# Performance work log

Hardware: AMD Instinct MI355X
Metric: run time of the kernel (lower is better)

Reference implementation:

```python
import jax, jax.numpy as jnp
import numpy as np

C = 128      # in_channels == out_channels
K = 3        # kernel_size
PAD = 1
DIL = 1
EPS = 1e-5


def setup_inputs() -> dict:
    key = jax.random.key(0)
    ks = jax.random.split(key, 6)
    B, L = 8, 16384
    x = jax.random.normal(ks[0], (B, C, L), jnp.float32)
    # depthwise Conv1d(C, C, K, groups=C), bias=True (nn.Conv1d default)
    dw_w = jax.random.normal(ks[1], (C, 1, K), jnp.float32) * (1.0 / np.sqrt(K))
    dw_b = jax.random.normal(ks[2], (C,), jnp.float32) * 0.05
    # LayerNorm(C)
    ln_g = jnp.ones((C,), jnp.float32)
    ln_b = jnp.zeros((C,), jnp.float32)
    # offset Linear(C -> groups*K) ; weight stored [out, in] like torch
    off_w = jax.random.normal(ks[3], (K, C), jnp.float32) * 0.02
    off_b = jnp.zeros((K,), jnp.float32)
    # deformable conv weight [C_out, C_in, K], bias=False
    dc_w = jax.random.normal(ks[4], (C, C, K), jnp.float32) * (1.0 / np.sqrt(C * K))
    return dict(x=x, dw_w=dw_w, dw_b=dw_b, ln_g=ln_g, ln_b=ln_b,
                off_w=off_w, off_b=off_b, dc_w=dc_w)


def _forward(x, dw_w, dw_b, ln_g, ln_b, off_w, off_b, dc_w):
    B, _, L = x.shape
    # --- dw_conv: depthwise conv + LayerNorm(channel) + ReLU ---
    y = jax.lax.conv_general_dilated(
        x, dw_w, window_strides=(1,), padding=[(PAD, PAD)],
        dimension_numbers=('NCH', 'OIH', 'NCH'), feature_group_count=C)
    y = y + dw_b[None, :, None]
    yt = y.transpose(0, 2, 1)                      # [B, L, C]
    mu = jnp.mean(yt, axis=-1, keepdims=True)
    var = jnp.mean((yt - mu) ** 2, axis=-1, keepdims=True)
    yn = (yt - mu) * jax.lax.rsqrt(var + EPS) * ln_g + ln_b
    yr = jax.nn.relu(yn)                           # [B, L, C]
    # --- offset linear: [B, L, C] -> [B, L, K] ---
    offset = yr @ off_w.T + off_b                  # [B, L, K]
    # --- deformable conv1d with linear interpolation, zero padding ---
    base = (jnp.arange(L, dtype=x.dtype)[None, :, None]
            + (jnp.arange(K, dtype=x.dtype) * DIL - PAD)[None, None, :])
    pos = base + offset                            # [B, L, K] fractional positions
    p0 = jnp.floor(pos)
    frac = pos - p0                                # [B, L, K]
    p0i = p0.astype(jnp.int32)
    p1i = p0i + 1
    v0 = ((p0i >= 0) & (p0i < L)).astype(x.dtype)
    v1 = ((p1i >= 0) & (p1i < L)).astype(x.dtype)
    i0 = jnp.clip(p0i, 0, L - 1)
    i1 = jnp.clip(p1i, 0, L - 1)
    gather = jax.vmap(lambda xb, ib: xb[:, ib])    # xb [C,L], ib [L,K] -> [C,L,K]
    g0 = gather(x, i0)                             # [B, C, L, K]
    g1 = gather(x, i1)
    g = g0 * ((1.0 - frac) * v0)[:, None] + g1 * (frac * v1)[:, None]
    # weighted sum over input channels and kernel taps
    return jnp.einsum('bclk,ock->bol', g, dc_w)    # [B, C_out, L]


def reference(x, dw_w, dw_b, ln_g, ln_b, off_w, off_b, dc_w):
    return _forward(x, dw_w, dw_b, ln_g, ln_b, off_w, off_b, dc_w)
```

## Files before the change

### kernel.cpp

```cpp
#include <hip/hip_runtime.h>
#include <hip/hip_bf16.h>
#include <cstdint>
#include <cstddef>

#define C_CH 128
#define L_LEN 16384
#define B_N 8
#define K_T 3
#define EPS 1e-5f
#define WPAD 8
#define WIN_G 144

typedef __attribute__((ext_vector_type(8))) short short8;
typedef __attribute__((ext_vector_type(4))) float float4v;

__device__ __forceinline__ short f2bf(float f) {
  union { float f; unsigned u; } v; v.f = f;
  unsigned r = v.u + 0x7fffu + ((v.u >> 16) & 1u);
  return (short)(r >> 16);
}
__device__ __forceinline__ float bflo(unsigned d) {
  union { unsigned u; float f; } v; v.u = d << 16; return v.f;
}
__device__ __forceinline__ float bfhi(unsigned d) {
  union { unsigned u; float f; } v; v.u = d & 0xffff0000u; return v.f;
}
__device__ __forceinline__ unsigned packbf(float a, float b) {
  unsigned ua = __float_as_uint(a) + 0x8000u;
  unsigned ub = __float_as_uint(b) + 0x8000u;
  return (ua >> 16) | (ub & 0xffff0000u);
}
__device__ __forceinline__ int clampL(int v) {
  return v < 0 ? 0 : (v > L_LEN - 1 ? L_LEN - 1 : v);
}
__device__ __forceinline__ void gl_lds16(const void* g, void* l) {
  __builtin_amdgcn_global_load_lds(
      (const __attribute__((address_space(1))) unsigned*)g,
      (__attribute__((address_space(3))) unsigned*)l, 16, 0, 0);
}

__global__ void repack_w2(const float* __restrict__ dc_w, short* __restrict__ Wp2) {
  int tid = blockIdx.x * 256 + threadIdx.x;
  if (tid >= C_CH * C_CH * K_T) return;
  int j = tid & 7;
  int m = (tid >> 3) & 127;
  int qk = (tid >> 10) & 3;
  int ks = tid >> 12;
  int kt = ks >> 2, s = ks & 3;
  int c = qk * 32 + s * 8 + j;
  Wp2[tid] = f2bf(dc_w[(m * C_CH + c) * K_T + kt]);
}

__global__ __launch_bounds__(256, 4) void offsets_k3(
    const float* __restrict__ x,
    const float* __restrict__ dw_w, const float* __restrict__ dw_b,
    const float* __restrict__ ln_g, const float* __restrict__ ln_b,
    const float* __restrict__ off_w, const float* __restrict__ off_b,
    short* __restrict__ xT, unsigned* __restrict__ d_wab, unsigned* __restrict__ d_idx) {
  __shared__ float swt[1152];
  int t = threadIdx.x;
  int b = blockIdx.y;
  int l0 = blockIdx.x * 64;

  for (int i = t; i < 1152; i += 256) {
    float v;
    if (i < 384) v = dw_w[i];
    else if (i < 512) v = dw_b[i - 384];
    else if (i < 640) v = ln_g[i - 512];
    else if (i < 768) v = ln_b[i - 640];
    else v = off_w[i - 768];
    swt[i] = v;
  }
  __syncthreads();

  int l_loc = t >> 2, sub = t & 3;
  int lg = l0 + l_loc;
  float mL = (lg >= 1) ? 1.f : 0.f;
  float mR = (lg + 1 < L_LEN) ? 1.f : 0.f;
  int lgm = lg - 1 < 0 ? 0 : lg - 1;
  int lgp = lg + 1 > L_LEN - 1 ? L_LEN - 1 : lg + 1;
  const float* xb = x + (size_t)b * C_CH * L_LEN;
  const float* xc = xb + (size_t)(sub * 32) * L_LEN;

  float ys[32];
  unsigned xpk[16];
  float sum = 0.f, sumsq = 0.f;
  #pragma unroll
  for (int j = 0; j < 32; ++j) {
    const float* xr = xc + (size_t)j * L_LEN;
    float xm = xr[lgm], x0 = xr[lg], xp = xr[lgp];
    int c = sub * 32 + j;
    float y = swt[384 + c] + mL * xm * swt[3 * c] + x0 * swt[3 * c + 1] + mR * xp * swt[3 * c + 2];
    ys[j] = y;
    sum += y;
    sumsq += y * y;
    unsigned ub = __float_as_uint(x0) + 0x8000u;
    if (j & 1) xpk[j >> 1] |= ub & 0xffff0000u;
    else       xpk[j >> 1]  = ub >> 16;
  }
  {
    short* xtp = xT + ((size_t)(b * L_LEN + lg) * C_CH + sub * 32);
    #pragma unroll
    for (int q4 = 0; q4 < 4; ++q4) {
      uint4 q;
      q.x = xpk[q4 * 4]; q.y = xpk[q4 * 4 + 1]; q.z = xpk[q4 * 4 + 2]; q.w = xpk[q4 * 4 + 3];
      *(uint4*)(xtp + q4 * 8) = q;
    }
  }
  sum += __shfl_xor(sum, 1, 64);     sum += __shfl_xor(sum, 2, 64);
  sumsq += __shfl_xor(sumsq, 1, 64); sumsq += __shfl_xor(sumsq, 2, 64);
  float mean = sum * (1.f / C_CH);
  float var = sumsq * (1.f / C_CH) - mean * mean;
  float rstd = rsqrtf(var + EPS);

  float o0 = 0.f, o1 = 0.f, o2 = 0.f;
  #pragma unroll
  for (int j = 0; j < 32; ++j) {
    int c = sub * 32 + j;
    float yn = (ys[j] - mean) * rstd * swt[512 + c] + swt[640 + c];
    float yr = yn > 0.f ? yn : 0.f;
    o0 += yr * swt[768 + c];
    o1 += yr * swt[896 + c];
    o2 += yr * swt[1024 + c];
  }
  o0 += __shfl_xor(o0, 1, 64); o0 += __shfl_xor(o0, 2, 64);
  o1 += __shfl_xor(o1, 1, 64); o1 += __shfl_xor(o1, 2, 64);
  o2 += __shfl_xor(o2, 1, 64); o2 += __shfl_xor(o2, 2, 64);

  if (sub < 3) {
    float o = (sub == 0 ? o0 : (sub == 1 ? o1 : o2)) + off_b[sub];
    float pos = (float)(lg + sub - 1) + o;
    float p0f = floorf(pos);
    float fr = pos - p0f;
    int i0 = (int)p0f, i1 = i0 + 1;
    float wa = (i0 >= 0 && i0 < L_LEN) ? (1.f - fr) : 0.f;
    float wbv = (i1 >= 0 && i1 < L_LEN) ? fr : 0.f;
    int i0c = clampL(i0), i1c = clampL(i1);
    size_t di = ((size_t)b * K_T + sub) * L_LEN + lg;
    d_wab[di] = packbf(wa, wbv);
    d_idx[di] = (unsigned)i0c | ((unsigned)i1c << 16);
  }
}

__global__ __launch_bounds__(256, 4) void deform_gemm3(
    const short* __restrict__ xT,
    const unsigned* __restrict__ d_wab, const unsigned* __restrict__ d_idx,
    const short* __restrict__ Wp2, float* __restrict__ out) {
  __shared__ short xs[WIN_G * 128];
  __shared__ unsigned s_wab[K_T][128];
  __shared__ unsigned s_r01[K_T][128];

  int t = threadIdx.x;
  int b = blockIdx.y;
  int l0 = blockIdx.x * 128;
  int wb0 = l0 - WPAD;
  int lane = t & 63, wv = t >> 6;
  int qk = lane >> 4, hrow = lane & 15;

  const short* xTb = xT + (size_t)b * L_LEN * C_CH;
  #pragma unroll
  for (int i = 0; i < 9; ++i) {
    int rb = wv * 36 + i * 4;
    int r = rb + (lane >> 4);
    int lrow = clampL(wb0 + r);
    int slot = lane & 15;
    const short* g = xTb + (size_t)lrow * C_CH + ((slot ^ (r & 15)) << 3);
    gl_lds16(g, &xs[rb * 128]);
  }

  for (int d = t; d < 384; d += 256) {
    int n = d & 127, tap = d >> 7;
    size_t di = ((size_t)b * K_T + tap) * L_LEN + (l0 + n);
    unsigned wab = d_wab[di];
    unsigned ii = d_idx[di];
    int r0 = (int)(ii & 0xffffu) - wb0;
    int r1 = (int)(ii >> 16) - wb0;
    if ((unsigned)r0 >= WIN_G) { r0 = 0; wab &= 0xffff0000u; }
    if ((unsigned)r1 >= WIN_G) { r1 = 0; wab &= 0x0000ffffu; }
    s_wab[tap][n] = wab;
    s_r01[tap][n] = (unsigned)r0 | ((unsigned)r1 << 16);
  }
  __syncthreads();

  float4v acc[8][2];
  #pragma unroll
  for (int i = 0; i < 8; ++i) {
    acc[i][0] = (float4v){0.f, 0.f, 0.f, 0.f};
    acc[i][1] = (float4v){0.f, 0.f, 0.f, 0.f};
  }
  const short* wpb = Wp2 + qk * 1024 + hrow * 8;
  const char* xsb = (const char*)xs;

  #pragma unroll
  for (int kt = 0; kt < 3; ++kt) {
    float wa[2], wbv[2];
    int b0[2], m0_[2], b1[2], m1_[2];
    #pragma unroll
    for (int nt = 0; nt < 2; ++nt) {
      int n = wv * 32 + nt * 16 + hrow;
      unsigned wab = s_wab[kt][n];
      wa[nt] = bflo(wab);
      wbv[nt] = bfhi(wab);
      unsigned r01 = s_r01[kt][n];
      int r0 = r01 & 0xffff, r1 = r01 >> 16;
      b0[nt] = r0 * 256; m0_[nt] = r0 & 15;
      b1[nt] = r1 * 256; m1_[nt] = r1 & 15;
    }
    #pragma unroll
    for (int s = 0; s < 4; ++s) {
      int ks = kt * 4 + s;
      int ch = qk * 4 + s;
      short8 bfrag[2];
      #pragma unroll
      for (int nt = 0; nt < 2; ++nt) {
        uint4 q0 = *(const uint4*)(xsb + b0[nt] + ((ch ^ m0_[nt]) << 4));
        uint4 q1 = *(const uint4*)(xsb + b1[nt] + ((ch ^ m1_[nt]) << 4));
        const unsigned* q0u = (const unsigned*)&q0;
        const unsigned* q1u = (const unsigned*)&q1;
        union { unsigned u[4]; short8 s8; } bu;
        #pragma unroll
        for (int j = 0; j < 4; ++j) {
          float glo = wa[nt] * bflo(q0u[j]) + wbv[nt] * bflo(q1u[j]);
          float ghi = wa[nt] * bfhi(q0u[j]) + wbv[nt] * bfhi(q1u[j]);
          bu.u[j] = packbf(glo, ghi);
        }
        bfrag[nt] = bu.s8;
      }
      const short* wk = wpb + ks * 4096;
      #pragma unroll
      for (int mt = 0; mt < 8; ++mt) {
        short8 a = *(const short8*)(wk + mt * 128);
        acc[mt][0] = __builtin_amdgcn_mfma_f32_16x16x32_bf16(a, bfrag[0], acc[mt][0], 0, 0, 0);
        acc[mt][1] = __builtin_amdgcn_mfma_f32_16x16x32_bf16(a, bfrag[1], acc[mt][1], 0, 0, 0);
      }
    }
  }

  float* ob = out + (size_t)b * C_CH * L_LEN + l0;
  #pragma unroll
  for (int mt = 0; mt < 8; ++mt) {
    #pragma unroll
    for (int nt = 0; nt < 2; ++nt) {
      int col = wv * 32 + nt * 16 + hrow;
      #pragma unroll
      for (int r = 0; r < 4; ++r) {
        ob[(size_t)(mt * 16 + qk * 4 + r) * L_LEN + col] = acc[mt][nt][r];
      }
    }
  }
}

extern "C" void kernel_launch(void* const* d_in, const int* in_sizes, int n_in,
                              void* d_out, int out_size, void* d_ws, size_t ws_size,
                              hipStream_t stream) {
  const float* x    = (const float*)d_in[0];
  const float* dw_w = (const float*)d_in[1];
  const float* dw_b = (const float*)d_in[2];
  const float* ln_g = (const float*)d_in[3];
  const float* ln_b = (const float*)d_in[4];
  const float* off_w = (const float*)d_in[5];
  const float* off_b = (const float*)d_in[6];
  const float* dc_w = (const float*)d_in[7];
  float* out = (float*)d_out;

  char* ws = (char*)d_ws;
  short* xT = (short*)ws;
  short* Wp2 = (short*)(ws + 0x2000000);
  unsigned* d_wab = (unsigned*)(ws + 0x2018000);
  unsigned* d_idx = (unsigned*)(ws + 0x2198000);

  hipLaunchKernelGGL(repack_w2, dim3(192), dim3(256), 0, stream, dc_w, Wp2);
  hipLaunchKernelGGL(offsets_k3, dim3(L_LEN / 64, B_N), dim3(256), 0, stream,
                     x, dw_w, dw_b, ln_g, ln_b, off_w, off_b, xT, d_wab, d_idx);
  hipLaunchKernelGGL(deform_gemm3, dim3(L_LEN / 128, B_N), dim3(256), 0, stream,
                     xT, d_wab, d_idx, Wp2, out);
}
```

Baseline: 191.0 us.

## Stage x tile in LDS with vectorized loads before LN/offset computation

The offsets kernel now loads a 132-row x window for 128 positions with float4 global loads, converts it to bf16, and stores it transposed into swizzled LDS. The xT write and the depthwise conv then read from LDS, and the block handles two 64-position passes. This replaces the scattered per-thread scalar strided loads (three per channel) with coalesced vector loads. In exchange the depthwise conv now uses bf16-rounded x values, which lowers precision slightly, and the kernel uses more LDS, which may reduce occupancy.

```diff
diff --git a/kernel.cpp b/kernel.cpp
--- a/kernel.cpp
+++ b/kernel.cpp
@@ -10,6 +10,7 @@
 #define EPS 1e-5f
 #define WPAD 8
 #define WIN_G 144
+#define WIN_O 132
 
 typedef __attribute__((ext_vector_type(8))) short short8;
 typedef __attribute__((ext_vector_type(4))) float float4v;
@@ -51,16 +52,20 @@
   Wp2[tid] = f2bf(dc_w[(m * C_CH + c) * K_T + kt]);
 }
 
-__global__ __launch_bounds__(256, 4) void offsets_k3(
+__global__ __launch_bounds__(256, 4) void offsets_k4(
     const float* __restrict__ x,
     const float* __restrict__ dw_w, const float* __restrict__ dw_b,
     const float* __restrict__ ln_g, const float* __restrict__ ln_b,
     const float* __restrict__ off_w, const float* __restrict__ off_b,
     short* __restrict__ xT, unsigned* __restrict__ d_wab, unsigned* __restrict__ d_idx) {
+  __shared__ short xs[WIN_O * 128];
   __shared__ float swt[1152];
+
   int t = threadIdx.x;
   int b = blockIdx.y;
-  int l0 = blockIdx.x * 64;
+  int l0 = blockIdx.x * 128;
+  const float* xb = x + (size_t)b * C_CH * L_LEN;
+  char* xsb = (char*)xs;
 
   for (int i = t; i < 1152; i += 256) {
     float v;
@@ -71,74 +76,126 @@
     else v = off_w[i - 768];
     swt[i] = v;
   }
+
+  int lane = t & 63, wv = t >> 6;
+
+  {
+    int cc = wv * 4 + (lane >> 4);
+    int lqi = lane & 15;
+    #pragma unroll
+    for (int i = 0; i < 3; ++i) {
+      int lq = i * 16 + lqi;
+      if (lq < 33) {
+        int bl = l0 - 2 + lq * 4;
+        float fv[8][4];
+        if (bl >= 0 && bl + 3 <= L_LEN - 1) {
+          #pragma unroll
+          for (int j = 0; j < 8; ++j) {
+            float4 f = *(const float4*)(xb + (size_t)(cc * 8 + j) * L_LEN + bl);
+            fv[j][0] = f.x; fv[j][1] = f.y; fv[j][2] = f.z; fv[j][3] = f.w;
+          }
+        } else {
+          #pragma unroll
+          for (int j = 0; j < 8; ++j)
+            #pragma unroll
+            for (int k = 0; k < 4; ++k)
+              fv[j][k] = xb[(size_t)(cc * 8 + j) * L_LEN + clampL(bl + k)];
+        }
+        #pragma unroll
+        for (int k = 0; k < 4; ++k) {
+          int rr = lq * 4 + k;
+          uint4 q;
+          q.x = packbf(fv[0][k], fv[1][k]);
+          q.y = packbf(fv[2][k], fv[3][k]);
+          q.z = packbf(fv[4][k], fv[5][k]);
+          q.w = packbf(fv[6][k], fv[7][k]);
+          *(uint4*)(xsb + rr * 256 + ((cc ^ (rr & 15)) << 4)) = q;
+        }
+      }
+    }
+  }
   __syncthreads();
 
-  int l_loc = t >> 2, sub = t & 3;
-  int lg = l0 + l_loc;
-  float mL = (lg >= 1) ? 1.f : 0.f;
-  float mR = (lg + 1 < L_LEN) ? 1.f : 0.f;
-  int lgm = lg - 1 < 0 ? 0 : lg - 1;
-  int lgp = lg + 1 > L_LEN - 1 ? L_LEN - 1 : lg + 1;
-  const float* xb = x + (size_t)b * C_CH * L_LEN;
-  const float* xc = xb + (size_t)(sub * 32) * L_LEN;
-
-  float ys[32];
-  unsigned xpk[16];
-  float sum = 0.f, sumsq = 0.f;
-  #pragma unroll
-  for (int j = 0; j < 32; ++j) {
-    const float* xr = xc + (size_t)j * L_LEN;
-    float xm = xr[lgm], x0 = xr[lg], xp = xr[lgp];
-    int c = sub * 32 + j;
-    float y = swt[384 + c] + mL * xm * swt[3 * c] + x0 * swt[3 * c + 1] + mR * xp * swt[3 * c + 2];
-    ys[j] = y;
-    sum += y;
-    sumsq += y * y;
-    unsigned ub = __float_as_uint(x0) + 0x8000u;
-    if (j & 1) xpk[j >> 1] |= ub & 0xffff0000u;
-    else       xpk[j >> 1]  = ub >> 16;
-  }
   {
-    short* xtp = xT + ((size_t)(b * L_LEN + lg) * C_CH + sub * 32);
-    #pragma unroll
-    for (int q4 = 0; q4 < 4; ++q4) {
-      uint4 q;
-      q.x = xpk[q4 * 4]; q.y = xpk[q4 * 4 + 1]; q.z = xpk[q4 * 4 + 2]; q.w = xpk[q4 * 4 + 3];
-      *(uint4*)(xtp + q4 * 8) = q;
-    }
-  }
-  sum += __shfl_xor(sum, 1, 64);     sum += __shfl_xor(sum, 2, 64);
-  sumsq += __shfl_xor(sumsq, 1, 64); sumsq += __shfl_xor(sumsq, 2, 64);
-  float mean = sum * (1.f / C_CH);
-  float var = sumsq * (1.f / C_CH) - mean * mean;
-  float rstd = rsqrtf(var + EPS);
-
-  float o0 = 0.f, o1 = 0.f, o2 = 0.f;
-  #pragma unroll
-  for (int j = 0; j < 32; ++j) {
-    int c = sub * 32 + j;
-    float yn = (ys[j] - mean) * rstd * swt[512 + c] + swt[640 + c];
-    float yr = yn > 0.f ? yn : 0.f;
-    o0 += yr * swt[768 + c];
-    o1 += yr * swt[896 + c];
-    o2 += yr * swt[1024 + c];
-  }
-  o0 += __shfl_xor(o0, 1, 64); o0 += __shfl_xor(o0, 2, 64);
-  o1 += __shfl_xor(o1, 1, 64); o1 += __shfl_xor(o1, 2, 64);
-  o2 += __shfl_xor(o2, 1, 64); o2 += __shfl_xor(o2, 2, 64);
-
-  if (sub < 3) {
-    float o = (sub == 0 ? o0 : (sub == 1 ? o1 : o2)) + off_b[sub];
-    float pos = (float)(lg + sub - 1) + o;
-    float p0f = floorf(pos);
-    float fr = pos - p0f;
-    int i0 = (int)p0f, i1 = i0 + 1;
-    float wa = (i0 >= 0 && i0 < L_LEN) ? (1.f - fr) : 0.f;
-    float wbv = (i1 >= 0 && i1 < L_LEN) ? fr : 0.f;
-    int i0c = clampL(i0), i1c = clampL(i1);
-    size_t di = ((size_t)b * K_T + sub) * L_LEN + lg;
-    d_wab[di] = packbf(wa, wbv);
-    d_idx[di] = (unsigned)i0c | ((unsigned)i1c << 16);
+    short* xTb = xT + (size_t)b * L_LEN * C_CH;
+    int sg = lane & 15;
+    int rbase = wv * 4 + (lane >> 4);
+    #pragma unroll
+    for (int i = 0; i < 8; ++i) {
+      int lr = rbase + i * 16;
+      int r = lr + 2;
+      uint4 q = *(const uint4*)(xsb + r * 256 + ((sg ^ (r & 15)) << 4));
+      *(uint4*)(xTb + (size_t)(l0 + lr) * C_CH + sg * 8) = q;
+    }
+  }
+
+  #pragma unroll
+  for (int it = 0; it < 2; ++it) {
+    int l_loc = (t >> 2) + it * 64;
+    int sub = t & 3;
+    int lg = l0 + l_loc;
+    float mL = (lg >= 1) ? 1.f : 0.f;
+    float mR = (lg + 1 < L_LEN) ? 1.f : 0.f;
+    int rm = l_loc + 2;
+
+    float ys[32];
+    float sum = 0.f, sumsq = 0.f;
+    #pragma unroll
+    for (int oct = 0; oct < 4; ++oct) {
+      int ch = sub * 4 + oct;
+      int r0 = rm - 1, r1 = rm, r2 = rm + 1;
+      uint4 q0 = *(const uint4*)(xsb + r0 * 256 + ((ch ^ (r0 & 15)) << 4));
+      uint4 q1 = *(const uint4*)(xsb + r1 * 256 + ((ch ^ (r1 & 15)) << 4));
+      uint4 q2 = *(const uint4*)(xsb + r2 * 256 + ((ch ^ (r2 & 15)) << 4));
+      const unsigned* u0 = (const unsigned*)&q0;
+      const unsigned* u1 = (const unsigned*)&q1;
+      const unsigned* u2 = (const unsigned*)&q2;
+      #pragma unroll
+      for (int j = 0; j < 4; ++j) {
+        int c = ch * 8 + 2 * j;
+        float y0 = swt[384 + c] + mL * bflo(u0[j]) * swt[3 * c]
+                 + bflo(u1[j]) * swt[3 * c + 1] + mR * bflo(u2[j]) * swt[3 * c + 2];
+        float y1 = swt[385 + c] + mL * bfhi(u0[j]) * swt[3 * c + 3]
+                 + bfhi(u1[j]) * swt[3 * c + 4] + mR * bfhi(u2[j]) * swt[3 * c + 5];
+        ys[oct * 8 + 2 * j] = y0;
+        ys[oct * 8 + 2 * j + 1] = y1;
+        sum += y0 + y1;
+        sumsq += y0 * y0 + y1 * y1;
+      }
+    }
+    sum += __shfl_xor(sum, 1, 64);     sum += __shfl_xor(sum, 2, 64);
+    sumsq += __shfl_xor(sumsq, 1, 64); sumsq += __shfl_xor(sumsq, 2, 64);
+    float mean = sum * (1.f / C_CH);
+    float var = sumsq * (1.f / C_CH) - mean * mean;
+    float rstd = rsqrtf(var + EPS);
+
+    float o0 = 0.f, o1 = 0.f, o2 = 0.f;
+    #pragma unroll
+    for (int li = 0; li < 32; ++li) {
+      int c = sub * 32 + li;
+      float yn = (ys[li] - mean) * rstd * swt[512 + c] + swt[640 + c];
+      float yr = yn > 0.f ? yn : 0.f;
+      o0 += yr * swt[768 + c];
+      o1 += yr * swt[896 + c];
+      o2 += yr * swt[1024 + c];
+    }
+    o0 += __shfl_xor(o0, 1, 64); o0 += __shfl_xor(o0, 2, 64);
+    o1 += __shfl_xor(o1, 1, 64); o1 += __shfl_xor(o1, 2, 64);
+    o2 += __shfl_xor(o2, 1, 64); o2 += __shfl_xor(o2, 2, 64);
+
+    if (sub < 3) {
+      float o = (sub == 0 ? o0 : (sub == 1 ? o1 : o2)) + off_b[sub];
+      float pos = (float)(lg + sub - 1) + o;
+      float p0f = floorf(pos);
+      float fr = pos - p0f;
+      int i0 = (int)p0f, i1 = i0 + 1;
+      float wa = (i0 >= 0 && i0 < L_LEN) ? (1.f - fr) : 0.f;
+      float wbv = (i1 >= 0 && i1 < L_LEN) ? fr : 0.f;
+      int i0c = clampL(i0), i1c = clampL(i1);
+      size_t di = ((size_t)b * K_T + sub) * L_LEN + lg;
+      d_wab[di] = packbf(wa, wbv);
+      d_idx[di] = (unsigned)i0c | ((unsigned)i1c << 16);
+    }
   }
 }
 
@@ -270,7 +327,7 @@
   unsigned* d_idx = (unsigned*)(ws + 0x2198000);
 
   hipLaunchKernelGGL(repack_w2, dim3(192), dim3(256), 0, stream, dc_w, Wp2);
-  hipLaunchKernelGGL(offsets_k3, dim3(L_LEN / 64, B_N), dim3(256), 0, stream,
+  hipLaunchKernelGGL(offsets_k4, dim3(L_LEN / 128, B_N), dim3(256), 0, stream,
                      x, dw_w, dw_b, ln_g, ln_b, off_w, off_b, xT, d_wab, d_idx);
   hipLaunchKernelGGL(deform_gemm3, dim3(L_LEN / 128, B_N), dim3(256), 0, stream,
                      xT, d_wab, d_idx, Wp2, out);
```

Result: no change. 189.5 us (-0.8%).
